# Optimization experiments

Measured on AMD Instinct MI355X. Metric: run time of the kernel, lower is better.

Reference implementation:

```python
import jax, jax.numpy as jnp
import numpy as np


def setup_inputs() -> dict:
    key = jax.random.key(0)
    k1, k2, k3, k4, k5, k6 = jax.random.split(key, 6)
    n_vars = 1000000
    n_constrs = 500000
    nnz = 20000000
    pred = jax.random.normal(k1, (n_vars,), dtype=jnp.float32)
    constr_idx = jax.random.randint(k2, (nnz,), 0, n_constrs, dtype=jnp.int32)
    var_idx = jax.random.randint(k3, (nnz,), 0, n_vars, dtype=jnp.int32)
    coeff = jax.random.normal(k4, (nnz,), dtype=jnp.float32)
    constr_rhs = jax.random.normal(k5, (n_constrs,), dtype=jnp.float32)
    constr_sense = jax.random.randint(k6, (n_constrs,), 1, 4, dtype=jnp.int32)  # 1=<=, 2=>=, 3===
    return {
        "pred": pred,
        "constr_idx": constr_idx,
        "var_idx": var_idx,
        "coeff": coeff,
        "constr_rhs": constr_rhs,
        "constr_sense": constr_sense,
        "n_vars": n_vars,
        "n_constrs": n_constrs,
    }


def reference(pred, constr_idx, var_idx, coeff, constr_rhs, constr_sense, n_vars, n_constrs):
    # probs = sigmoid(pred); ax[i] = sum over nnz entries of coeff * probs[var_idx]
    probs = jax.nn.sigmoid(pred)
    contrib = coeff * probs[var_idx]                      # [nnz]
    ax = jax.ops.segment_sum(contrib, constr_idx, num_segments=n_constrs)  # [n_constrs]
    le = jax.nn.relu(ax - constr_rhs)      # sense == 1 (<=)
    ge = jax.nn.relu(constr_rhs - ax)      # sense == 2 (>=)
    eq = jnp.abs(ax - constr_rhs)          # sense == 3 (==)
    violations = jnp.where(constr_sense == 1, le,
                  jnp.where(constr_sense == 2, ge,
                   jnp.where(constr_sense == 3, eq, jnp.zeros_like(ax))))
    return violations.mean()  # reduction='mean'
```

## Files before the change

kernel.cpp:

```cpp
#include <hip/hip_runtime.h>
#include <math.h>

#define R_LOG2 13
#define R_BKT  8192
#define SLICE  16
#define MAXNB  64
#define PB     512
#define BLK_RECS 8192

typedef int      iv4 __attribute__((ext_vector_type(4)));
typedef float    fv4 __attribute__((ext_vector_type(4)));
typedef unsigned uv4 __attribute__((ext_vector_type(4)));


__global__ void init_fast(const float4* __restrict__ pred4,
                          float4* __restrict__ probs4,
                          unsigned* __restrict__ cursor,
                          float* __restrict__ out,
                          int n_vars4, int nb) {
    int i = blockIdx.x * blockDim.x + threadIdx.x;
    if (i < n_vars4) {
        float4 p = pred4[i];
        float4 q;
        q.x = 1.0f / (1.0f + expf(-p.x));
        q.y = 1.0f / (1.0f + expf(-p.y));
        q.z = 1.0f / (1.0f + expf(-p.z));
        q.w = 1.0f / (1.0f + expf(-p.w));
        probs4[i] = q;
    }
    if (i < nb) cursor[i] = 0;
    if (i == 0) out[0] = 0.0f;
}

__global__ __launch_bounds__(PB) void partition_kernel(
        const int* __restrict__ cidx, const int* __restrict__ vidx,
        const float* __restrict__ coeff, const float* __restrict__ probs,
        unsigned* __restrict__ cursor, unsigned* __restrict__ recs,
        int nnz4, int nb, unsigned cap) {
    __shared__ unsigned sorted[BLK_RECS];
    __shared__ unsigned hist[8 * MAXNB];
    __shared__ unsigned lcur[8 * MAXNB];
    __shared__ unsigned bst[MAXNB + 1];
    __shared__ unsigned gbs[MAXNB];

    const int tid  = threadIdx.x;
    const int w    = tid >> 6;
    const int lane = tid & 63;

    hist[tid] = 0;

    unsigned rw[16];
    unsigned bk[16];
    bool     gv[4];
    const unsigned vbase = blockIdx.x * (BLK_RECS / 4);
    const bool full = (vbase + (BLK_RECS / 4)) <= (unsigned)nnz4;

    if (full) {
        #pragma unroll
        for (int g = 0; g < 4; ++g) {
            unsigned v = vbase + g * PB + (unsigned)tid;
            iv4 c4 = __builtin_nontemporal_load((const iv4*)cidx + v);
            iv4 v4 = __builtin_nontemporal_load((const iv4*)vidx + v);
            fv4 w4 = __builtin_nontemporal_load((const fv4*)coeff + v);
            int   cc[4] = {c4.x, c4.y, c4.z, c4.w};
            float vv[4] = {w4.x * probs[v4.x], w4.y * probs[v4.y],
                           w4.z * probs[v4.z], w4.w * probs[v4.w]};
            #pragma unroll
            for (int j = 0; j < 4; ++j) {
                int k = g * 4 + j;
                unsigned bits = __builtin_bit_cast(unsigned, vv[j]);
                bits += 0x7FFFu + ((bits >> 16) & 1u);
                rw[k] = ((unsigned)(cc[j] & (R_BKT - 1)) << 16) | (bits >> 16);
                bk[k] = (unsigned)cc[j] >> R_LOG2;
            }
            gv[g] = true;
        }
    } else {
        #pragma unroll
        for (int g = 0; g < 4; ++g) {
            unsigned v = vbase + g * PB + (unsigned)tid;
            gv[g] = v < (unsigned)nnz4;
            if (gv[g]) {
                int4   c4 = ((const int4*)cidx)[v];
                int4   v4 = ((const int4*)vidx)[v];
                float4 w4 = ((const float4*)coeff)[v];
                int   cc[4] = {c4.x, c4.y, c4.z, c4.w};
                float vv[4] = {w4.x * probs[v4.x], w4.y * probs[v4.y],
                               w4.z * probs[v4.z], w4.w * probs[v4.w]};
                #pragma unroll
                for (int j = 0; j < 4; ++j) {
                    int k = g * 4 + j;
                    unsigned bits = __builtin_bit_cast(unsigned, vv[j]);
                    bits += 0x7FFFu + ((bits >> 16) & 1u);
                    rw[k] = ((unsigned)(cc[j] & (R_BKT - 1)) << 16) | (bits >> 16);
                    bk[k] = (unsigned)cc[j] >> R_LOG2;
                }
            }
        }
    }
    __syncthreads();

    if (full) {
        #pragma unroll
        for (int k = 0; k < 16; ++k)
            atomicAdd(&hist[(w << 6) + bk[k]], 1u);
    } else {
        #pragma unroll
        for (int g = 0; g < 4; ++g) if (gv[g]) {
            #pragma unroll
            for (int j = 0; j < 4; ++j)
                atomicAdd(&hist[(w << 6) + bk[g * 4 + j]], 1u);
        }
    }
    __syncthreads();

    if (w == 0) {
        unsigned h[8];
        unsigned cnt = 0;
        if (lane < nb) {
            #pragma unroll
            for (int j = 0; j < 8; ++j) { h[j] = hist[(j << 6) + lane]; cnt += h[j]; }
        }
        unsigned sc = cnt;
        #pragma unroll
        for (int d = 1; d < 64; d <<= 1) {
            unsigned t = __shfl_up(sc, d, 64);
            if (lane >= d) sc += t;
        }
        unsigned excl  = sc - cnt;
        unsigned total = __shfl(sc, nb - 1, 64);
        if (lane < nb) {
            bst[lane] = excl;
            unsigned run = excl;
            #pragma unroll
            for (int j = 0; j < 8; ++j) { lcur[(j << 6) + lane] = run; run += h[j]; }
            gbs[lane] = cnt ? atomicAdd(&cursor[lane], cnt) : 0u;
        }
        if (lane == 0) bst[nb] = total;
    }
    __syncthreads();

    if (full) {
        #pragma unroll
        for (int k = 0; k < 16; ++k) {
            unsigned pos = atomicAdd(&lcur[(w << 6) + bk[k]], 1u);
            sorted[pos] = rw[k];
        }
    } else {
        #pragma unroll
        for (int g = 0; g < 4; ++g) if (gv[g]) {
            #pragma unroll
            for (int j = 0; j < 4; ++j) {
                int k = g * 4 + j;
                unsigned pos = atomicAdd(&lcur[(w << 6) + bk[k]], 1u);
                sorted[pos] = rw[k];
            }
        }
    }
    __syncthreads();

    for (int b = w; b < nb; b += 8) {
        unsigned st = bst[b], en = bst[b + 1], gb = gbs[b];
        unsigned* dst = recs + (size_t)b * cap;
        for (unsigned p = st + (unsigned)lane; p < en; p += 64u) {
            unsigned pos = gb + (p - st);
            if (pos < cap) __builtin_nontemporal_store(sorted[p], &dst[pos]);
        }
    }
}

__global__ __launch_bounds__(256) void accum_kernel(
        const unsigned* __restrict__ recs, const unsigned* __restrict__ cursor,
        float* __restrict__ partial, int n_constrs, unsigned cap) {
    __shared__ float acc[R_BKT];
    const int b = blockIdx.x / SLICE;
    const int s = blockIdx.x % SLICE;
    for (int j = threadIdx.x * 4; j < R_BKT; j += blockDim.x * 4)
        *(float4*)(acc + j) = make_float4(0.f, 0.f, 0.f, 0.f);
    __syncthreads();

    unsigned cnt = cursor[b];
    if (cnt > cap) cnt = cap;
    const unsigned* base = recs + (size_t)b * cap;

    unsigned c4 = cnt >> 2;
    unsigned s4 = (unsigned)(((unsigned long long)c4 * s) / SLICE);
    unsigned e4 = (unsigned)(((unsigned long long)c4 * (s + 1)) / SLICE);
    const uv4* b4 = (const uv4*)base;
    #pragma unroll 2
    for (unsigned i = s4 + threadIdx.x; i < e4; i += blockDim.x) {
        uv4 r = __builtin_nontemporal_load(b4 + i);
        unsafeAtomicAdd(&acc[r.x >> 16], __builtin_bit_cast(float, (r.x & 0xFFFFu) << 16));
        unsafeAtomicAdd(&acc[r.y >> 16], __builtin_bit_cast(float, (r.y & 0xFFFFu) << 16));
        unsafeAtomicAdd(&acc[r.z >> 16], __builtin_bit_cast(float, (r.z & 0xFFFFu) << 16));
        unsafeAtomicAdd(&acc[r.w >> 16], __builtin_bit_cast(float, (r.w & 0xFFFFu) << 16));
    }
    if (s == SLICE - 1) {
        for (unsigned i = (c4 << 2) + threadIdx.x; i < cnt; i += blockDim.x) {
            unsigned r = base[i];
            unsafeAtomicAdd(&acc[r >> 16], __builtin_bit_cast(float, (r & 0xFFFFu) << 16));
        }
    }
    __syncthreads();

    const int gb = b * R_BKT;
    float* dst = partial + (size_t)s * n_constrs;
    for (int j = threadIdx.x * 4; j < R_BKT; j += blockDim.x * 4) {
        int g = gb + j;
        if (g < n_constrs) {
            fv4 v = {acc[j], acc[j+1], acc[j+2], acc[j+3]};
            __builtin_nontemporal_store(v, (fv4*)(dst + g));
        }
    }
}

__device__ __forceinline__ float viol(float d, int sn) {
    return (sn == 1) ? fmaxf(d, 0.0f)
         : (sn == 2) ? fmaxf(-d, 0.0f)
         : (sn == 3) ? fabsf(d)
         : 0.0f;
}

__global__ void reduce_fast(const float* __restrict__ partial,
                            const float4* __restrict__ rhs4,
                            const int4* __restrict__ sense4,
                            float* __restrict__ out,
                            int n4, float inv_n) {
    int i = blockIdx.x * blockDim.x + threadIdx.x;
    float v = 0.0f;
    if (i < n4) {
        fv4 a = {0.f, 0.f, 0.f, 0.f};
        const fv4* p4 = (const fv4*)partial;
        #pragma unroll
        for (int s = 0; s < SLICE; ++s) {
            fv4 p = __builtin_nontemporal_load(p4 + (size_t)s * n4 + i);
            a.x += p.x; a.y += p.y; a.z += p.z; a.w += p.w;
        }
        float4 r = rhs4[i];
        int4  sn = sense4[i];
        v = viol(a.x - r.x, sn.x) + viol(a.y - r.y, sn.y)
          + viol(a.z - r.z, sn.z) + viol(a.w - r.w, sn.w);
    }
    #pragma unroll
    for (int off = 32; off > 0; off >>= 1)
        v += __shfl_down(v, off, 64);
    __shared__ float wsum[4];
    int lane = threadIdx.x & 63;
    int wid  = threadIdx.x >> 6;
    if (lane == 0) wsum[wid] = v;
    __syncthreads();
    if (threadIdx.x == 0)
        atomicAdd(out, (wsum[0] + wsum[1] + wsum[2] + wsum[3]) * inv_n);
}


__global__ void init_kernel(const float* __restrict__ pred,
                            float* __restrict__ probs,
                            float* __restrict__ ax,
                            float* __restrict__ out,
                            int n_vars, int n_constrs) {
    int i = blockIdx.x * blockDim.x + threadIdx.x;
    if (i < n_vars) probs[i] = 1.0f / (1.0f + expf(-pred[i]));
    if (i < n_constrs) ax[i] = 0.0f;
    if (i == 0) out[0] = 0.0f;
}

__global__ void scatter_kernel(const int* __restrict__ cidx,
                               const int* __restrict__ vidx,
                               const float* __restrict__ coeff,
                               const float* __restrict__ probs,
                               float* __restrict__ ax,
                               int nnz) {
    int i = blockIdx.x * blockDim.x + threadIdx.x;
    long long base = (long long)i * 4;
    if (base + 3 < (long long)nnz) {
        int4   c = ((const int4*)cidx)[i];
        int4   v = ((const int4*)vidx)[i];
        float4 w = ((const float4*)coeff)[i];
        unsafeAtomicAdd(&ax[c.x], w.x * probs[v.x]);
        unsafeAtomicAdd(&ax[c.y], w.y * probs[v.y]);
        unsafeAtomicAdd(&ax[c.z], w.z * probs[v.z]);
        unsafeAtomicAdd(&ax[c.w], w.w * probs[v.w]);
    } else if (base < (long long)nnz) {
        for (long long k = base; k < (long long)nnz; ++k)
            unsafeAtomicAdd(&ax[cidx[k]], coeff[k] * probs[vidx[k]]);
    }
}

__global__ void reduce_kernel(const float* __restrict__ ax,
                              const float* __restrict__ rhs,
                              const int* __restrict__ sense,
                              float* __restrict__ out,
                              int n_constrs, float inv_n) {
    int i = blockIdx.x * blockDim.x + threadIdx.x;
    float v = 0.0f;
    if (i < n_constrs) {
        float d = ax[i] - rhs[i];
        int s = sense[i];
        v = (s == 1) ? fmaxf(d, 0.0f)
          : (s == 2) ? fmaxf(-d, 0.0f)
          : (s == 3) ? fabsf(d)
          : 0.0f;
    }
    #pragma unroll
    for (int off = 32; off > 0; off >>= 1)
        v += __shfl_down(v, off, 64);
    __shared__ float wsum[4];
    int lane = threadIdx.x & 63;
    int wid  = threadIdx.x >> 6;
    if (lane == 0) wsum[wid] = v;
    __syncthreads();
    if (threadIdx.x == 0)
        atomicAdd(out, (wsum[0] + wsum[1] + wsum[2] + wsum[3]) * inv_n);
}


static inline size_t align16(size_t x) { return (x + 15) & ~(size_t)15; }

extern "C" void kernel_launch(void* const* d_in, const int* in_sizes, int n_in,
                              void* d_out, int out_size, void* d_ws, size_t ws_size,
                              hipStream_t stream) {
    const float* pred  = (const float*)d_in[0];
    const int*   cidx  = (const int*)d_in[1];
    const int*   vidx  = (const int*)d_in[2];
    const float* coeff = (const float*)d_in[3];
    const float* rhs   = (const float*)d_in[4];
    const int*   sense = (const int*)d_in[5];

    const int n_vars    = in_sizes[0];
    const int nnz       = in_sizes[1];
    const int n_constrs = in_sizes[4];
    const int B = 256;
    const float inv_n = 1.0f / (float)n_constrs;

    const int nb = (n_constrs + R_BKT - 1) / R_BKT;
    unsigned cap = (unsigned)(((double)nnz * R_BKT / (double)n_constrs) * 1.0625) + 1024;
    cap = (cap + 3u) & ~3u;

    size_t off_probs  = 0;
    size_t off_cursor = align16(off_probs + (size_t)n_vars * 4);
    size_t off_recs   = align16(off_cursor + (size_t)nb * 4);
    size_t off_part   = align16(off_recs + (size_t)nb * cap * 4);
    size_t need_fast  = off_part + (size_t)SLICE * n_constrs * 4;

    bool fast = (ws_size >= need_fast) && (nb <= MAXNB) && ((nnz & 3) == 0)
             && ((n_vars & 3) == 0) && ((n_constrs & 3) == 0);

    if (fast) {
        float*    probs   = (float*)((char*)d_ws + off_probs);
        unsigned* cursor  = (unsigned*)((char*)d_ws + off_cursor);
        unsigned* recs    = (unsigned*)((char*)d_ws + off_recs);
        float*    partial = (float*)((char*)d_ws + off_part);
        float*    out     = (float*)d_out;

        int n_vars4 = n_vars >> 2;
        int init_n  = n_vars4 > nb ? n_vars4 : nb;
        init_fast<<<(init_n + B - 1) / B, B, 0, stream>>>(
            (const float4*)pred, (float4*)probs, cursor, out, n_vars4, nb);

        int nnz4 = nnz >> 2;
        int nblk1 = (nnz4 + (BLK_RECS / 4) - 1) / (BLK_RECS / 4);
        partition_kernel<<<nblk1, PB, 0, stream>>>(
            cidx, vidx, coeff, probs, cursor, recs, nnz4, nb, cap);

        accum_kernel<<<nb * SLICE, B, 0, stream>>>(
            recs, cursor, partial, n_constrs, cap);

        int n4 = n_constrs >> 2;
        reduce_fast<<<(n4 + B - 1) / B, B, 0, stream>>>(
            partial, (const float4*)rhs, (const int4*)sense,
            out, n4, inv_n);
    } else {
        float* probs = (float*)d_ws;
        float* ax    = probs + n_vars;
        float* out   = (float*)d_out;

        int init_n = n_vars > n_constrs ? n_vars : n_constrs;
        init_kernel<<<(init_n + B - 1) / B, B, 0, stream>>>(
            pred, probs, ax, out, n_vars, n_constrs);

        int n_vec_threads = (nnz + 3) / 4;
        scatter_kernel<<<(n_vec_threads + B - 1) / B, B, 0, stream>>>(
            cidx, vidx, coeff, probs, ax, nnz);

        reduce_kernel<<<(n_constrs + B - 1) / B, B, 0, stream>>>(
            ax, rhs, sense, out, n_constrs, inv_n);
    }
}
```

Measured before the change: 460.8 us.

## Store probs as bf16 and merge slice partials via global atomics

The sigmoid probabilities are now stored as bf16, which halves the gather table so random probs lookups hit cache more often. Accumulation blocks now atomically add their shared-memory sums into a single ax array (zeroed in init) instead of writing SLICE separate partial arrays. The slice count drops from 16 to 8. This cuts partial-array writes and reads in the final reduce, but adds global float atomics, lowers accumulate parallelism, and makes the sum order nondeterministic.

Result: faster. 447.4 us (-2.9%).

```diff
diff --git a/kernel.cpp b/kernel.cpp
--- a/kernel.cpp
+++ b/kernel.cpp
@@ -3,7 +3,7 @@
 
 #define R_LOG2 13
 #define R_BKT  8192
-#define SLICE  16
+#define SLICE  8
 #define MAXNB  64
 #define PB     512
 #define BLK_RECS 8192
@@ -12,29 +12,37 @@
 typedef float    fv4 __attribute__((ext_vector_type(4)));
 typedef unsigned uv4 __attribute__((ext_vector_type(4)));
 
+__device__ __forceinline__ unsigned short f32_to_bf16_rne(float f) {
+    unsigned b = __builtin_bit_cast(unsigned, f);
+    b += 0x7FFFu + ((b >> 16) & 1u);
+    return (unsigned short)(b >> 16);
+}
+
 
 __global__ void init_fast(const float4* __restrict__ pred4,
-                          float4* __restrict__ probs4,
+                          ushort4* __restrict__ probs4,
+                          float4* __restrict__ ax4,
                           unsigned* __restrict__ cursor,
                           float* __restrict__ out,
-                          int n_vars4, int nb) {
+                          int n_vars4, int nc4, int nb) {
     int i = blockIdx.x * blockDim.x + threadIdx.x;
     if (i < n_vars4) {
         float4 p = pred4[i];
-        float4 q;
-        q.x = 1.0f / (1.0f + expf(-p.x));
-        q.y = 1.0f / (1.0f + expf(-p.y));
-        q.z = 1.0f / (1.0f + expf(-p.z));
-        q.w = 1.0f / (1.0f + expf(-p.w));
+        ushort4 q;
+        q.x = f32_to_bf16_rne(1.0f / (1.0f + expf(-p.x)));
+        q.y = f32_to_bf16_rne(1.0f / (1.0f + expf(-p.y)));
+        q.z = f32_to_bf16_rne(1.0f / (1.0f + expf(-p.z)));
+        q.w = f32_to_bf16_rne(1.0f / (1.0f + expf(-p.w)));
         probs4[i] = q;
     }
+    if (i < nc4) ax4[i] = make_float4(0.f, 0.f, 0.f, 0.f);
     if (i < nb) cursor[i] = 0;
     if (i == 0) out[0] = 0.0f;
 }
 
 __global__ __launch_bounds__(PB) void partition_kernel(
         const int* __restrict__ cidx, const int* __restrict__ vidx,
-        const float* __restrict__ coeff, const float* __restrict__ probs,
+        const float* __restrict__ coeff, const unsigned short* __restrict__ probs,
         unsigned* __restrict__ cursor, unsigned* __restrict__ recs,
         int nnz4, int nb, unsigned cap) {
     __shared__ unsigned sorted[BLK_RECS];
@@ -63,8 +71,11 @@
             iv4 v4 = __builtin_nontemporal_load((const iv4*)vidx + v);
             fv4 w4 = __builtin_nontemporal_load((const fv4*)coeff + v);
             int   cc[4] = {c4.x, c4.y, c4.z, c4.w};
-            float vv[4] = {w4.x * probs[v4.x], w4.y * probs[v4.y],
-                           w4.z * probs[v4.z], w4.w * probs[v4.w]};
+            float vv[4] = {
+                w4.x * __builtin_bit_cast(float, (unsigned)probs[v4.x] << 16),
+                w4.y * __builtin_bit_cast(float, (unsigned)probs[v4.y] << 16),
+                w4.z * __builtin_bit_cast(float, (unsigned)probs[v4.z] << 16),
+                w4.w * __builtin_bit_cast(float, (unsigned)probs[v4.w] << 16)};
             #pragma unroll
             for (int j = 0; j < 4; ++j) {
                 int k = g * 4 + j;
@@ -85,8 +96,11 @@
                 int4   v4 = ((const int4*)vidx)[v];
                 float4 w4 = ((const float4*)coeff)[v];
                 int   cc[4] = {c4.x, c4.y, c4.z, c4.w};
-                float vv[4] = {w4.x * probs[v4.x], w4.y * probs[v4.y],
-                               w4.z * probs[v4.z], w4.w * probs[v4.w]};
+                float vv[4] = {
+                    w4.x * __builtin_bit_cast(float, (unsigned)probs[v4.x] << 16),
+                    w4.y * __builtin_bit_cast(float, (unsigned)probs[v4.y] << 16),
+                    w4.z * __builtin_bit_cast(float, (unsigned)probs[v4.z] << 16),
+                    w4.w * __builtin_bit_cast(float, (unsigned)probs[v4.w] << 16)};
                 #pragma unroll
                 for (int j = 0; j < 4; ++j) {
                     int k = g * 4 + j;
@@ -171,7 +185,7 @@
 
 __global__ __launch_bounds__(256) void accum_kernel(
         const unsigned* __restrict__ recs, const unsigned* __restrict__ cursor,
-        float* __restrict__ partial, int n_constrs, unsigned cap) {
+        float* __restrict__ ax, int n_constrs, unsigned cap) {
     __shared__ float acc[R_BKT];
     const int b = blockIdx.x / SLICE;
     const int s = blockIdx.x % SLICE;
@@ -204,13 +218,10 @@
     __syncthreads();
 
     const int gb = b * R_BKT;
-    float* dst = partial + (size_t)s * n_constrs;
-    for (int j = threadIdx.x * 4; j < R_BKT; j += blockDim.x * 4) {
+    for (int j = threadIdx.x; j < R_BKT; j += blockDim.x) {
         int g = gb + j;
-        if (g < n_constrs) {
-            fv4 v = {acc[j], acc[j+1], acc[j+2], acc[j+3]};
-            __builtin_nontemporal_store(v, (fv4*)(dst + g));
-        }
+        if (g < n_constrs)
+            unsafeAtomicAdd(&ax[g], acc[j]);
     }
 }
 
@@ -221,7 +232,7 @@
          : 0.0f;
 }
 
-__global__ void reduce_fast(const float* __restrict__ partial,
+__global__ void reduce_fast(const float4* __restrict__ ax4,
                             const float4* __restrict__ rhs4,
                             const int4* __restrict__ sense4,
                             float* __restrict__ out,
@@ -229,13 +240,7 @@
     int i = blockIdx.x * blockDim.x + threadIdx.x;
     float v = 0.0f;
     if (i < n4) {
-        fv4 a = {0.f, 0.f, 0.f, 0.f};
-        const fv4* p4 = (const fv4*)partial;
-        #pragma unroll
-        for (int s = 0; s < SLICE; ++s) {
-            fv4 p = __builtin_nontemporal_load(p4 + (size_t)s * n4 + i);
-            a.x += p.x; a.y += p.y; a.z += p.z; a.w += p.w;
-        }
+        float4 a = ax4[i];
         float4 r = rhs4[i];
         int4  sn = sense4[i];
         v = viol(a.x - r.x, sn.x) + viol(a.y - r.y, sn.y)
@@ -338,25 +343,28 @@
     cap = (cap + 3u) & ~3u;
 
     size_t off_probs  = 0;
-    size_t off_cursor = align16(off_probs + (size_t)n_vars * 4);
+    size_t off_cursor = align16(off_probs + (size_t)n_vars * 2);
     size_t off_recs   = align16(off_cursor + (size_t)nb * 4);
-    size_t off_part   = align16(off_recs + (size_t)nb * cap * 4);
-    size_t need_fast  = off_part + (size_t)SLICE * n_constrs * 4;
+    size_t off_ax     = align16(off_recs + (size_t)nb * cap * 4);
+    size_t need_fast  = off_ax + (size_t)n_constrs * 4;
 
     bool fast = (ws_size >= need_fast) && (nb <= MAXNB) && ((nnz & 3) == 0)
              && ((n_vars & 3) == 0) && ((n_constrs & 3) == 0);
 
     if (fast) {
-        float*    probs   = (float*)((char*)d_ws + off_probs);
-        unsigned* cursor  = (unsigned*)((char*)d_ws + off_cursor);
-        unsigned* recs    = (unsigned*)((char*)d_ws + off_recs);
-        float*    partial = (float*)((char*)d_ws + off_part);
-        float*    out     = (float*)d_out;
+        unsigned short* probs  = (unsigned short*)((char*)d_ws + off_probs);
+        unsigned*       cursor = (unsigned*)((char*)d_ws + off_cursor);
+        unsigned*       recs   = (unsigned*)((char*)d_ws + off_recs);
+        float*          ax     = (float*)((char*)d_ws + off_ax);
+        float*          out    = (float*)d_out;
 
         int n_vars4 = n_vars >> 2;
-        int init_n  = n_vars4 > nb ? n_vars4 : nb;
+        int nc4     = n_constrs >> 2;
+        int init_n  = n_vars4 > nc4 ? n_vars4 : nc4;
+        if (init_n < nb) init_n = nb;
         init_fast<<<(init_n + B - 1) / B, B, 0, stream>>>(
-            (const float4*)pred, (float4*)probs, cursor, out, n_vars4, nb);
+            (const float4*)pred, (ushort4*)probs, (float4*)ax, cursor, out,
+            n_vars4, nc4, nb);
 
         int nnz4 = nnz >> 2;
         int nblk1 = (nnz4 + (BLK_RECS / 4) - 1) / (BLK_RECS / 4);
@@ -364,12 +372,11 @@
             cidx, vidx, coeff, probs, cursor, recs, nnz4, nb, cap);
 
         accum_kernel<<<nb * SLICE, B, 0, stream>>>(
-            recs, cursor, partial, n_constrs, cap);
-
-        int n4 = n_constrs >> 2;
-        reduce_fast<<<(n4 + B - 1) / B, B, 0, stream>>>(
-            partial, (const float4*)rhs, (const int4*)sense,
-            out, n4, inv_n);
+            recs, cursor, ax, n_constrs, cap);
+
+        reduce_fast<<<(nc4 + B - 1) / B, B, 0, stream>>>(
+            (const float4*)ax, (const float4*)rhs, (const int4*)sense,
+            out, nc4, inv_n);
     } else {
         float* probs = (float*)d_ws;
         float* ax    = probs + n_vars;
```
